# Kernel optimization log

Measured on AMD Instinct MI355X. Metric: run time of the kernel, lower is better.

The kernel has to match this reference:

```python
import jax, jax.numpy as jnp
import numpy as np

H = 1024       # hidden_size
NH = 16        # num heads
HD = H // NH   # head dim
EPS = 1e-12


def setup_inputs() -> dict:
    key = jax.random.key(0)
    ks = jax.random.split(key, 12)
    s = 1.0 / np.sqrt(H)
    return {
        "hidden_states": jax.random.normal(ks[0], (2, 2048, H), jnp.float32),
        "attention_mask": jnp.zeros((2, 1, 1, 2048), jnp.float32),
        "wq": jax.random.uniform(ks[1], (H, H), jnp.float32, -s, s),
        "bq": jnp.zeros((H,), jnp.float32),
        "wk": jax.random.uniform(ks[2], (H, H), jnp.float32, -s, s),
        "bk": jnp.zeros((H,), jnp.float32),
        "wv": jax.random.uniform(ks[3], (H, H), jnp.float32, -s, s),
        "bv": jnp.zeros((H,), jnp.float32),
        "wo": jax.random.uniform(ks[4], (H, H), jnp.float32, -s, s),
        "bo": jnp.zeros((H,), jnp.float32),
        "ln_gamma": jnp.ones((H,), jnp.float32),
        "ln_beta": jnp.zeros((H,), jnp.float32),
    }


def reference(hidden_states, attention_mask, wq, bq, wk, bk, wv, bv, wo, bo, ln_gamma, ln_beta):
    residual = hidden_states
    # pre-LayerNorm
    mu = jnp.mean(hidden_states, axis=-1, keepdims=True)
    var = jnp.var(hidden_states, axis=-1, keepdims=True)
    x = (hidden_states - mu) / jnp.sqrt(var + EPS) * ln_gamma + ln_beta

    B, S, _ = x.shape
    # QKV projections (torch Linear: x @ W.T + b), split heads -> [B, NH, S, HD]
    def proj(w, b):
        return (x @ w.T + b).reshape(B, S, NH, HD).transpose(0, 2, 1, 3)
    q = proj(wq, bq)
    k = proj(wk, bk)
    v = proj(wv, bv)

    scores = jnp.einsum("bhqd,bhkd->bhqk", q, k) / np.sqrt(HD).astype(np.float32)
    scores = scores + attention_mask  # broadcast additive mask
    probs = jax.nn.softmax(scores, axis=-1)
    ctx = jnp.einsum("bhqk,bhkd->bhqd", probs, v)
    ctx = ctx.transpose(0, 2, 1, 3).reshape(B, S, NH * HD)

    out = ctx @ wo.T + bo
    return out + residual
```

## Files before the change

### kernel.cpp

```cpp
#include <hip/hip_runtime.h>
#include <cstdint>

typedef unsigned short u16;
typedef __bf16  bf16x8 __attribute__((ext_vector_type(8)));
typedef unsigned short u16x8 __attribute__((ext_vector_type(8)));
typedef unsigned short u16x4 __attribute__((ext_vector_type(4)));
typedef float   f32x4  __attribute__((ext_vector_type(4)));

#define LOG2E 1.44269504088896340736f

__device__ __forceinline__ u16 f2b(float f) {
  union { __bf16 h; u16 u; } c; c.h = (__bf16)f;
  return c.u;
}

__device__ __forceinline__ int swz(int row) { return (row & 7) ^ ((row >> 3) & 7); }
__device__ __forceinline__ int sidx(int row, int k) {
  return row * 64 + ((((k >> 3) ^ swz(row)) & 7) << 3) + (k & 7);
}
__device__ __forceinline__ bf16x8 ld_frag(const u16* base, int row, int k) {
  return *(const bf16x8*)(base + sidx(row, k));
}

__device__ __forceinline__ void async16(const u16* g, u16* l) {
  __builtin_amdgcn_global_load_lds(
      (__attribute__((address_space(1))) unsigned int*)(uintptr_t)g,
      (__attribute__((address_space(3))) unsigned int*)(uintptr_t)l,
      16, 0, 0);
}

__global__ __launch_bounds__(256) void cvt_kernel(
    const float* __restrict__ w0, const float* __restrict__ w1,
    const float* __restrict__ w2, const float* __restrict__ w3,
    u16* __restrict__ dst) {
  const float* src = (blockIdx.y == 0) ? w0 : (blockIdx.y == 1) ? w1
                   : (blockIdx.y == 2) ? w2 : w3;
  const int idx = (blockIdx.x * 256 + threadIdx.x) * 4;
  f32x4 v = *(const f32x4*)(src + idx);
  u16x4 o;
#pragma unroll
  for (int j = 0; j < 4; ++j) o[j] = f2b(v[j]);
  *(u16x4*)(dst + (size_t)blockIdx.y * 1048576 + idx) = o;
}

__global__ __launch_bounds__(256) void ln_kernel(
    const float* __restrict__ hs, const float* __restrict__ gamma,
    const float* __restrict__ beta, u16* __restrict__ X) {
  __shared__ float red[8];
  const int row = blockIdx.x;
  const int tid = threadIdx.x;
  f32x4 v = *(const f32x4*)(hs + (size_t)row * 1024 + tid * 4);
  float s = 0.f, s2 = 0.f;
#pragma unroll
  for (int j = 0; j < 4; ++j) { s += v[j]; s2 += v[j] * v[j]; }
#pragma unroll
  for (int o = 1; o < 64; o <<= 1) { s += __shfl_xor(s, o); s2 += __shfl_xor(s2, o); }
  const int wid = tid >> 6, lane = tid & 63;
  if (lane == 0) { red[wid] = s; red[4 + wid] = s2; }
  __syncthreads();
  s  = red[0] + red[1] + red[2] + red[3];
  s2 = red[4] + red[5] + red[6] + red[7];
  const float mean = s * (1.f / 1024.f);
  const float var  = fmaxf(s2 * (1.f / 1024.f) - mean * mean, 0.f);
  const float rstd = rsqrtf(var + 1e-12f);
  f32x4 g = *(const f32x4*)(gamma + tid * 4);
  f32x4 bb = *(const f32x4*)(beta + tid * 4);
  u16x4 outv;
#pragma unroll
  for (int j = 0; j < 4; ++j) outv[j] = f2b((v[j] - mean) * rstd * g[j] + bb[j]);
  *(u16x4*)(X + (size_t)row * 1024 + tid * 4) = outv;
}

template <int MODE>
__device__ __forceinline__ void gemm_tile_128(
    const u16* __restrict__ A, const u16* __restrict__ Bt,
    const float* __restrict__ bias, const float* __restrict__ res,
    void* __restrict__ Cv, int ldc, int m0, int nG) {
  __shared__ __align__(16) u16 As[128 * 64];
  __shared__ __align__(16) u16 Bs[128 * 64];
  const int tid = threadIdx.x;
  const int wid = tid >> 6;
  const int lane = tid & 63;
  const int l15 = lane & 15, lq = lane >> 4;
  const int wm = (wid & 1) << 6, wn = (wid >> 1) << 6;
  const int srow = tid >> 3;
  const int sg = tid & 7;

  f32x4 acc[4][4] = {};

  for (int k0 = 0; k0 < 1024; k0 += 64) {
#pragma unroll
    for (int i = 0; i < 4; ++i) {
      int row = (i << 5) + srow;
      int kc  = k0 + (((sg ^ swz(row)) & 7) << 3);
      async16(A + (size_t)row * 1024 + kc, As + (i << 11) + (wid << 9));
    }
#pragma unroll
    for (int i = 0; i < 4; ++i) {
      int row = (i << 5) + srow;
      int kc  = k0 + (((sg ^ swz(row)) & 7) << 3);
      async16(Bt + (size_t)row * 1024 + kc, Bs + (i << 11) + (wid << 9));
    }
    __syncthreads();
#pragma unroll
    for (int kk = 0; kk < 2; ++kk) {
      bf16x8 af[4], bf[4];
#pragma unroll
      for (int mi = 0; mi < 4; ++mi) af[mi] = ld_frag(As, wm + (mi << 4) + l15, (kk << 5) + (lq << 3));
#pragma unroll
      for (int ni = 0; ni < 4; ++ni) bf[ni] = ld_frag(Bs, wn + (ni << 4) + l15, (kk << 5) + (lq << 3));
#pragma unroll
      for (int mi = 0; mi < 4; ++mi)
#pragma unroll
        for (int ni = 0; ni < 4; ++ni)
          acc[mi][ni] = __builtin_amdgcn_mfma_f32_16x16x32_bf16(af[mi], bf[ni], acc[mi][ni], 0, 0, 0);
    }
    __syncthreads();
  }

  if (MODE == 2) {
    u16* Rg = (wid < 2 ? As : Bs) + ((wid & 1) << 12);
#pragma unroll
    for (int ni = 0; ni < 4; ++ni) {
      const float bv = bias[wn + (ni << 4) + l15];
#pragma unroll
      for (int mi = 0; mi < 4; ++mi) {
        u16x4 pk;
#pragma unroll
        for (int r = 0; r < 4; ++r) pk[r] = f2b(acc[mi][ni][r] + bv);
        *(u16x4*)(Rg + sidx((ni << 4) + l15, (mi << 4) + (lq << 2))) = pk;
      }
    }
    __asm__ volatile("" ::: "memory");
    const int rrow = lane >> 3;
    const int rg8  = (lane & 7) << 3;
    const int mg0 = m0 + wm;
    const int bb = mg0 >> 11, ss0 = mg0 & 2047;
    const int hh = (nG + wn) >> 6;
    u16* vbase = (u16*)Cv + ((size_t)((bb << 4) + hh) * 64) * 2048 + ss0;
#pragma unroll
    for (int p = 0; p < 8; ++p) {
      const int nl = (p << 3) + rrow;
      bf16x8 rowv = ld_frag(Rg, nl, rg8);
      *(bf16x8*)(vbase + (size_t)nl * 2048 + rg8) = rowv;
    }
  } else {
#pragma unroll
    for (int ni = 0; ni < 4; ++ni) {
      const int n = wn + (ni << 4) + l15;
      const float bv = bias[n];
#pragma unroll
      for (int mi = 0; mi < 4; ++mi) {
#pragma unroll
        for (int r = 0; r < 4; ++r) {
          const int m = wm + (mi << 4) + (lq << 2) + r;
          float v = acc[mi][ni][r] + bv;
          if (MODE == 1) {
            v += res[(size_t)m * ldc + n];
            ((float*)Cv)[(size_t)m * ldc + n] = v;
          } else {
            ((u16*)Cv)[(size_t)m * ldc + n] = f2b(v);
          }
        }
      }
    }
  }
}

__global__ __launch_bounds__(256, 3) void qkv_kernel(
    const u16* __restrict__ X, const u16* __restrict__ W,
    const float* __restrict__ bq, const float* __restrict__ bk, const float* __restrict__ bv,
    u16* __restrict__ QK, u16* __restrict__ VT) {
  const int n0 = blockIdx.x << 7;
  const int m0 = blockIdx.y << 7;
  const int wsel = n0 >> 10;
  const int nloc = n0 & 1023;
  const u16* Bt = W + (size_t)wsel * 1048576 + (size_t)nloc * 1024;
  if (wsel < 2) {
    const float* bias = (wsel == 0 ? bq : bk) + nloc;
    gemm_tile_128<0>(X + (size_t)m0 * 1024, Bt, bias, nullptr,
                     QK + (size_t)m0 * 2048 + n0, 2048, 0, 0);
  } else {
    gemm_tile_128<2>(X + (size_t)m0 * 1024, Bt, bv + nloc, nullptr,
                     VT, 0, m0, nloc);
  }
}

__global__ __launch_bounds__(256, 3) void out_kernel(
    const u16* __restrict__ CTX, const u16* __restrict__ wo,
    const float* __restrict__ bo, const float* __restrict__ res, float* __restrict__ OUT) {
  const int n0 = blockIdx.x << 7;
  const int m0 = blockIdx.y << 7;
  gemm_tile_128<1>(CTX + (size_t)m0 * 1024, wo + (size_t)n0 * 1024, bo + n0,
                   res + (size_t)m0 * 1024 + n0, OUT + (size_t)m0 * 1024 + n0, 1024, 0, 0);
}

__global__ __launch_bounds__(256, 2) void attn_kernel(
    const u16* __restrict__ QK, const u16* __restrict__ VT,
    const float* __restrict__ mask, u16* __restrict__ CTX) {
  __shared__ __align__(16) u16 Ksb[2][64 * 64];
  __shared__ __align__(16) u16 Vtsb[2][64 * 64];
  __shared__ __align__(16) u16 Ps[4 * 32 * 64];
  const int tid = threadIdx.x;
  const int wid = tid >> 6;
  const int lane = tid & 63;
  const int l15 = lane & 15, lq = lane >> 4;
  const int qt = blockIdx.x, h = blockIdx.y, b = blockIdx.z;

  const int qbase = (b << 11) + (qt << 7) + (wid << 5);
  const u16* Kbase  = QK + (size_t)(b << 11) * 2048 + 1024 + (h << 6);
  const u16* VTbase = VT + (size_t)(((b << 4) + h) << 6) * 2048;

  bf16x8 qf[2][2];
#pragma unroll
  for (int f = 0; f < 2; ++f)
#pragma unroll
    for (int kc = 0; kc < 2; ++kc)
      qf[f][kc] = *(const bf16x8*)(QK + (size_t)(qbase + (f << 4) + l15) * 2048 + (h << 6) + (kc << 5) + (lq << 3));

  f32x4 cacc[2][4] = {};
  float l_run[2] = {0.f, 0.f};

  const int sg = lane & 7;
  const int srow0 = (wid << 4) + (lane >> 3);
  const int srow1 = srow0 + 8;
  const int gk0 = ((sg ^ swz(srow0)) & 7) << 3;
  const int gk1 = ((sg ^ swz(srow1)) & 7) << 3;
  const int ld0 = ((wid << 1) + 0) << 9;
  const int ld1 = ((wid << 1) + 1) << 9;
  u16* Pw = Ps + (wid << 11);

  async16(Kbase + (size_t)srow0 * 2048 + gk0, &Ksb[0][0] + ld0);
  async16(Kbase + (size_t)srow1 * 2048 + gk1, &Ksb[0][0] + ld1);
  async16(VTbase + (size_t)srow0 * 2048 + gk0, &Vtsb[0][0] + ld0);
  async16(VTbase + (size_t)srow1 * 2048 + gk1, &Vtsb[0][0] + ld1);

  for (int kt = 0; kt < 32; ++kt) {
    const u16* Ks  = &Ksb[kt & 1][0];
    const u16* Vts = &Vtsb[kt & 1][0];
    __syncthreads();
    if (kt + 1 < 32) {
      const int nk = (kt + 1) << 6;
      async16(Kbase + (size_t)(nk + srow0) * 2048 + gk0, &Ksb[(kt + 1) & 1][0] + ld0);
      async16(Kbase + (size_t)(nk + srow1) * 2048 + gk1, &Ksb[(kt + 1) & 1][0] + ld1);
      async16(VTbase + (size_t)srow0 * 2048 + nk + gk0, &Vtsb[(kt + 1) & 1][0] + ld0);
      async16(VTbase + (size_t)srow1 * 2048 + nk + gk1, &Vtsb[(kt + 1) & 1][0] + ld1);
    }

    f32x4 sacc[2][4] = {};
#pragma unroll
    for (int kc = 0; kc < 2; ++kc) {
      bf16x8 kf[4];
#pragma unroll
      for (int ki = 0; ki < 4; ++ki) kf[ki] = ld_frag(Ks, (ki << 4) + l15, (kc << 5) + (lq << 3));
#pragma unroll
      for (int f = 0; f < 2; ++f)
#pragma unroll
        for (int ki = 0; ki < 4; ++ki)
          sacc[f][ki] = __builtin_amdgcn_mfma_f32_16x16x32_bf16(kf[ki], qf[f][kc], sacc[f][ki], 0, 0, 0);
    }

    f32x4 mvl[4];
#pragma unroll
    for (int ki = 0; ki < 4; ++ki) {
      f32x4 mv = *(const f32x4*)(mask + (b << 11) + (kt << 6) + (ki << 4) + (lq << 2));
#pragma unroll
      for (int r = 0; r < 4; ++r) mvl[ki][r] = mv[r] * LOG2E;
    }

#pragma unroll
    for (int f = 0; f < 2; ++f) {
      float rs = 0.f;
#pragma unroll
      for (int ki = 0; ki < 4; ++ki) {
#pragma unroll
        for (int r = 0; r < 4; ++r) {
          float pv = __builtin_amdgcn_exp2f(sacc[f][ki][r] * (0.125f * LOG2E) + mvl[ki][r]);
          sacc[f][ki][r] = pv;
          rs += pv;
        }
      }
      l_run[f] += rs;
#pragma unroll
      for (int ki = 0; ki < 4; ++ki) {
        u16x4 pk;
#pragma unroll
        for (int r = 0; r < 4; ++r) pk[r] = f2b(sacc[f][ki][r]);
        *(u16x4*)(Pw + sidx((f << 4) + l15, (ki << 4) + (lq << 2))) = pk;
      }
    }
    __asm__ volatile("" ::: "memory");

#pragma unroll
    for (int kc = 0; kc < 2; ++kc) {
      bf16x8 pf[2];
#pragma unroll
      for (int f = 0; f < 2; ++f) pf[f] = ld_frag(Pw, (f << 4) + l15, (kc << 5) + (lq << 3));
#pragma unroll
      for (int dm = 0; dm < 4; ++dm) {
        bf16x8 vf = ld_frag(Vts, (dm << 4) + l15, (kc << 5) + (lq << 3));
#pragma unroll
        for (int f = 0; f < 2; ++f)
          cacc[f][dm] = __builtin_amdgcn_mfma_f32_16x16x32_bf16(vf, pf[f], cacc[f][dm], 0, 0, 0);
      }
    }
  }

#pragma unroll
  for (int f = 0; f < 2; ++f) {
    float rs = l_run[f];
    rs += __shfl_xor(rs, 16);
    rs += __shfl_xor(rs, 32);
    const float inv = 1.0f / rs;
    u16* Crow = CTX + (size_t)(qbase + (f << 4) + l15) * 1024 + (h << 6);
#pragma unroll
    for (int dm = 0; dm < 4; ++dm) {
      u16x4 o;
#pragma unroll
      for (int r = 0; r < 4; ++r) o[r] = f2b(cacc[f][dm][r] * inv);
      *(u16x4*)(Crow + (dm << 4) + (lq << 2)) = o;
    }
  }
}

extern "C" void kernel_launch(void* const* d_in, const int* in_sizes, int n_in,
                              void* d_out, int out_size, void* d_ws, size_t ws_size,
                              hipStream_t stream) {
  const float* hs   = (const float*)d_in[0];
  const float* mask = (const float*)d_in[1];
  const float* wq   = (const float*)d_in[2];
  const float* bq   = (const float*)d_in[3];
  const float* wk   = (const float*)d_in[4];
  const float* bk   = (const float*)d_in[5];
  const float* wv   = (const float*)d_in[6];
  const float* bv   = (const float*)d_in[7];
  const float* wo   = (const float*)d_in[8];
  const float* bo   = (const float*)d_in[9];
  const float* lg   = (const float*)d_in[10];
  const float* lb   = (const float*)d_in[11];

  u16* X   = (u16*)d_ws;
  u16* QK  = X + (size_t)4096 * 1024;
  u16* CTX = QK + (size_t)4096 * 2048;
  u16* W   = CTX + (size_t)4096 * 1024;
  u16* VT  = W + (size_t)4 * 1048576;
  float* OUT = (float*)d_out;

  ln_kernel<<<4096, 256, 0, stream>>>(hs, lg, lb, X);
  cvt_kernel<<<dim3(1024, 4), 256, 0, stream>>>(wq, wk, wv, wo, W);
  qkv_kernel<<<dim3(24, 32), 256, 0, stream>>>(X, W, bq, bk, bv, QK, VT);
  attn_kernel<<<dim3(16, 16, 2), 256, 0, stream>>>(QK, VT, mask, CTX);
  out_kernel<<<dim3(8, 32), 256, 0, stream>>>(CTX, W + (size_t)3 * 1048576, bo, hs, OUT);
}
```

Before: 226.3 us.

## Merge LN and weight cast kernels; register-prefetch GEMM tiles instead of async LDS loads

Combines the LayerNorm and weight-conversion kernels into a single launch, with extra blocks handling the bf16 weight casts, which saves one kernel launch. The GEMM main loop now reads the next K-tile into registers while MFMAs run on the current tile, then writes it to swizzled LDS, replacing direct global-to-LDS async loads followed by a barrier. This is meant to hide global load latency behind compute. The cost is more registers per thread and an extra LDS write pass, which may lower occupancy.

```diff
diff --git a/kernel.cpp b/kernel.cpp
--- a/kernel.cpp
+++ b/kernel.cpp
@@ -29,26 +29,27 @@
       16, 0, 0);
 }
 
-__global__ __launch_bounds__(256) void cvt_kernel(
+__global__ __launch_bounds__(256) void prep_kernel(
+    const float* __restrict__ hs, const float* __restrict__ gamma,
+    const float* __restrict__ beta, u16* __restrict__ X,
     const float* __restrict__ w0, const float* __restrict__ w1,
     const float* __restrict__ w2, const float* __restrict__ w3,
-    u16* __restrict__ dst) {
-  const float* src = (blockIdx.y == 0) ? w0 : (blockIdx.y == 1) ? w1
-                   : (blockIdx.y == 2) ? w2 : w3;
-  const int idx = (blockIdx.x * 256 + threadIdx.x) * 4;
-  f32x4 v = *(const f32x4*)(src + idx);
-  u16x4 o;
-#pragma unroll
-  for (int j = 0; j < 4; ++j) o[j] = f2b(v[j]);
-  *(u16x4*)(dst + (size_t)blockIdx.y * 1048576 + idx) = o;
-}
-
-__global__ __launch_bounds__(256) void ln_kernel(
-    const float* __restrict__ hs, const float* __restrict__ gamma,
-    const float* __restrict__ beta, u16* __restrict__ X) {
+    u16* __restrict__ Wd) {
+  const int tid = threadIdx.x;
+  if (blockIdx.x >= 4096) {
+    const int idx4 = blockIdx.x - 4096;
+    const int mat = idx4 >> 10;
+    const float* src = (mat == 0) ? w0 : (mat == 1) ? w1 : (mat == 2) ? w2 : w3;
+    const int idx = ((idx4 & 1023) * 256 + tid) * 4;
+    f32x4 v = *(const f32x4*)(src + idx);
+    u16x4 o;
+#pragma unroll
+    for (int j = 0; j < 4; ++j) o[j] = f2b(v[j]);
+    *(u16x4*)(Wd + (size_t)mat * 1048576 + idx) = o;
+    return;
+  }
   __shared__ float red[8];
   const int row = blockIdx.x;
-  const int tid = threadIdx.x;
   f32x4 v = *(const f32x4*)(hs + (size_t)row * 1024 + tid * 4);
   float s = 0.f, s2 = 0.f;
 #pragma unroll
@@ -87,21 +88,32 @@
   const int sg = tid & 7;
 
   f32x4 acc[4][4] = {};
+  u16x8 ar[4], br[4];
+
+#pragma unroll
+  for (int i = 0; i < 4; ++i) {
+    int row = (i << 5) + srow;
+    ar[i] = *(const u16x8*)(A  + (size_t)row * 1024 + (sg << 3));
+    br[i] = *(const u16x8*)(Bt + (size_t)row * 1024 + (sg << 3));
+  }
 
   for (int k0 = 0; k0 < 1024; k0 += 64) {
+    if (k0) __syncthreads();
 #pragma unroll
     for (int i = 0; i < 4; ++i) {
       int row = (i << 5) + srow;
-      int kc  = k0 + (((sg ^ swz(row)) & 7) << 3);
-      async16(A + (size_t)row * 1024 + kc, As + (i << 11) + (wid << 9));
-    }
-#pragma unroll
-    for (int i = 0; i < 4; ++i) {
-      int row = (i << 5) + srow;
-      int kc  = k0 + (((sg ^ swz(row)) & 7) << 3);
-      async16(Bt + (size_t)row * 1024 + kc, Bs + (i << 11) + (wid << 9));
+      *(u16x8*)(As + sidx(row, sg << 3)) = ar[i];
+      *(u16x8*)(Bs + sidx(row, sg << 3)) = br[i];
     }
     __syncthreads();
+    if (k0 + 64 < 1024) {
+#pragma unroll
+      for (int i = 0; i < 4; ++i) {
+        int row = (i << 5) + srow;
+        ar[i] = *(const u16x8*)(A  + (size_t)row * 1024 + k0 + 64 + (sg << 3));
+        br[i] = *(const u16x8*)(Bt + (size_t)row * 1024 + k0 + 64 + (sg << 3));
+      }
+    }
 #pragma unroll
     for (int kk = 0; kk < 2; ++kk) {
       bf16x8 af[4], bf[4];
@@ -115,8 +127,8 @@
         for (int ni = 0; ni < 4; ++ni)
           acc[mi][ni] = __builtin_amdgcn_mfma_f32_16x16x32_bf16(af[mi], bf[ni], acc[mi][ni], 0, 0, 0);
     }
-    __syncthreads();
-  }
+  }
+  __syncthreads();
 
   if (MODE == 2) {
     u16* Rg = (wid < 2 ? As : Bs) + ((wid & 1) << 12);
@@ -346,8 +358,7 @@
   u16* VT  = W + (size_t)4 * 1048576;
   float* OUT = (float*)d_out;
 
-  ln_kernel<<<4096, 256, 0, stream>>>(hs, lg, lb, X);
-  cvt_kernel<<<dim3(1024, 4), 256, 0, stream>>>(wq, wk, wv, wo, W);
+  prep_kernel<<<8192, 256, 0, stream>>>(hs, lg, lb, X, wq, wk, wv, wo, W);
   qkv_kernel<<<dim3(24, 32), 256, 0, stream>>>(X, W, bq, bk, bv, QK, VT);
   attn_kernel<<<dim3(16, 16, 2), 256, 0, stream>>>(QK, VT, mask, CTX);
   out_kernel<<<dim3(8, 32), 256, 0, stream>>>(CTX, W + (size_t)3 * 1048576, bo, hs, OUT);
```

Measured after the change: 209.1 us. 1.08x faster.
